# Optimization experiments

Measured on AMD Instinct MI355X. Metric: run time of the kernel, lower is better.

Reference implementation:

```python
import jax, jax.numpy as jnp
import numpy as np

B, S, H = 2, 2048, 4096
NH, HD = 32, 128          # num attention heads, head dim (kv_channels)
KVH = 2                   # multi_query_group_num (KV heads)
ROT = HD // 2             # 64 rotary dims -> rope cache last-2 dim = 32
QKV = NH * HD + 2 * KVH * HD  # 4608


def apply_rope(x, rope):
    # x: [b, nh, s, hd]; rope: [b, s, ROT//2, 2]
    b, nh, s, hd = x.shape
    x_rot, x_pass = x[..., :ROT], x[..., ROT:]
    xs = x_rot.reshape(b, nh, s, ROT // 2, 2)
    rc = rope[:, :s].reshape(b, 1, s, ROT // 2, 2)
    out = jnp.stack([
        xs[..., 0] * rc[..., 0] - xs[..., 1] * rc[..., 1],
        xs[..., 1] * rc[..., 0] + xs[..., 0] * rc[..., 1],
    ], axis=-1).reshape(b, nh, s, ROT)
    return jnp.concatenate([out, x_pass], axis=-1)


def setup_inputs() -> dict:
    key = jax.random.key(0)
    ks = jax.random.split(key, 6)
    hidden_states = jax.random.normal(ks[0], (B, S, H), dtype=jnp.float32)
    rotary_pos_emb = jax.random.normal(ks[1], (B, S, ROT // 2, 2), dtype=jnp.float32)
    # causal mask: True = masked (strict upper triangle), matching module's ~tril
    causal = jnp.triu(jnp.ones((S, S), dtype=jnp.bool_), k=1)
    attention_mask = jnp.broadcast_to(causal[None, None], (B, 1, S, S))
    W_qkv = jax.random.normal(ks[2], (QKV, H), dtype=jnp.float32) * (1.0 / np.sqrt(H))
    b_qkv = jax.random.normal(ks[3], (QKV,), dtype=jnp.float32) * 0.02
    W_dense = jax.random.normal(ks[4], (H, NH * HD), dtype=jnp.float32) * (1.0 / np.sqrt(NH * HD))
    return {"hidden_states": hidden_states, "rotary_pos_emb": rotary_pos_emb,
            "attention_mask": attention_mask, "W_qkv": W_qkv, "b_qkv": b_qkv,
            "W_dense": W_dense}


def reference(hidden_states, rotary_pos_emb, attention_mask, W_qkv, b_qkv, W_dense):
    b, s, _ = hidden_states.shape
    mixed = hidden_states @ W_qkv.T + b_qkv  # [b, s, QKV]
    q, k, v = jnp.split(mixed, [NH * HD, NH * HD + KVH * HD], axis=-1)
    q = q.reshape(b, s, NH, HD).transpose(0, 2, 1, 3)   # [b, NH, s, hd]
    k = k.reshape(b, s, KVH, HD).transpose(0, 2, 1, 3)  # [b, KVH, s, hd]
    v = v.reshape(b, s, KVH, HD).transpose(0, 2, 1, 3)
    q = apply_rope(q, rotary_pos_emb)
    k = apply_rope(k, rotary_pos_emb)
    # GQA expand KV heads to NH
    rep = NH // KVH
    k = jnp.repeat(k, rep, axis=1)
    v = jnp.repeat(v, rep, axis=1)
    scale = 1.0 / np.sqrt(HD)
    scores = jnp.einsum('bhqd,bhkd->bhqk', q, k).astype(jnp.float32) * scale
    scores = jnp.where(attention_mask, -jnp.inf, scores)
    probs = jax.nn.softmax(scores, axis=-1).astype(v.dtype)
    ctx = jnp.einsum('bhqk,bhkd->bhqd', probs, v)       # [b, NH, s, hd]
    ctx = ctx.transpose(0, 2, 1, 3).reshape(b, s, NH * HD)
    return ctx @ W_dense.T
```

## Files before the change

### kernel.cpp

```cpp
#include <hip/hip_runtime.h>
#include <hip/hip_bf16.h>
#include <stdint.h>

#define Bb 2
#define Ss 2048
#define Hh 4096
#define NHh 32
#define HDd 128
#define KVHh 2

typedef __attribute__((ext_vector_type(8))) short bf16x8;
typedef __attribute__((ext_vector_type(4))) float f32x4;
typedef __attribute__((ext_vector_type(16))) float f32x16;
typedef __attribute__((ext_vector_type(4))) unsigned int u32x4;
typedef unsigned short u16;
typedef unsigned int u32;
typedef unsigned long long u64;

__device__ __forceinline__ u16 f2b(float f) {
  union { float f; u32 u; } v; v.f = f;
  u32 r = v.u + 0x7fffu + ((v.u >> 16) & 1u);
  return (u16)(r >> 16);
}
__device__ __forceinline__ float b2f(u16 h) {
  union { u32 u; float f; } v; v.u = ((u32)h) << 16;
  return v.f;
}

__device__ __forceinline__ u32 cvtpk(float lo, float hi_) {
  u32 r;
  asm("v_cvt_pk_bf16_f32 %0, %1, %2" : "=v"(r) : "v"(lo), "v"(hi_));
  return r;
}
__device__ __forceinline__ void plswap(u32& x, u32& y) {
  asm volatile("v_permlane32_swap_b32 %0, %1" : "+v"(x), "+v"(y));
}

__device__ __forceinline__ void gload_lds16(const u16* g, u16* l) {
  __builtin_amdgcn_global_load_lds(
      (const __attribute__((address_space(1))) u32*)(uintptr_t)g,
      (__attribute__((address_space(3))) u32*)(u32)(uintptr_t)l,
      16, 0, 0);
}

__global__ void cvt2_k(const float* __restrict__ a, u16* __restrict__ oa,
                       const float* __restrict__ b, u16* __restrict__ ob) {
  int i = blockIdx.x * blockDim.x + threadIdx.x;
  const float* src;
  u16* dst;
  int off;
  if (i < 4194304) { src = a; dst = oa; off = i; }
  else { src = b; dst = ob; off = i - 4194304; }
  int idx = off * 4;
  float4 v = *(const float4*)&src[idx];
  u64 pack = (u64)f2b(v.x) | ((u64)f2b(v.y) << 16) |
             ((u64)f2b(v.z) << 32) | ((u64)f2b(v.w) << 48);
  *(u64*)&dst[idx] = pack;
}

__global__ void cvtW_k(const float* __restrict__ in, u16* __restrict__ out) {
  int i = blockIdx.x * blockDim.x + threadIdx.x;
  int idx = i * 4;
  float4 v = *(const float4*)&in[idx];
  u64 pack = (u64)f2b(v.x) | ((u64)f2b(v.y) << 16) |
             ((u64)f2b(v.z) << 32) | ((u64)f2b(v.w) << 48);
  *(u64*)&out[idx] = pack;
}

__global__ void rope_k(u16* __restrict__ X, const float* __restrict__ rope, int nheads) {
  int i = blockIdx.x * blockDim.x + threadIdx.x;
  int p = i & 31;
  int s = (i >> 5) & (Ss - 1);
  int bh = i >> 16;
  if (bh >= Bb * nheads) return;
  int b = bh / nheads;
  size_t base = ((size_t)bh * Ss + s) * HDd + p * 2;
  u32 x01 = *(u32*)&X[base];
  float x0 = b2f((u16)(x01 & 0xffff));
  float x1 = b2f((u16)(x01 >> 16));
  float2 rc = *(const float2*)&rope[(((size_t)b * Ss + s) * 32 + p) * 2];
  float o0 = x0 * rc.x - x1 * rc.y;
  float o1 = x1 * rc.x + x0 * rc.y;
  u32 o = (u32)f2b(o0) | ((u32)f2b(o1) << 16);
  *(u32*)&X[base] = o;
}

template <int KK>
__device__ __forceinline__ void stage_tileA(const u16* __restrict__ gbase, u16* dst, int tid) {
#pragma unroll
  for (int li = 0; li < 2; ++li) {
    int t16 = li * 512 + tid;
    int rt = t16 >> 2, ct = t16 & 3;
    int cg = ct ^ ((rt >> 1) & 3);
    gload_lds16(gbase + (size_t)rt * KK + cg * 8, dst + t16 * 8);
  }
}
template <int KK>
__device__ __forceinline__ void stage_tileB(const u16* __restrict__ gbase, u16* dst, int tid) {
  int t16 = tid;
  int rt = t16 >> 2, ct = t16 & 3;
  int cg = ct ^ ((rt >> 1) & 3);
  gload_lds16(gbase + (size_t)rt * KK + cg * 8, dst + t16 * 8);
}

__device__ __forceinline__ bf16x8 frag128(const u16* buf, int row, int lk) {
  int ch = lk ^ ((row >> 1) & 3);
  return *(const bf16x8*)&buf[row * 32 + ch * 8];
}

template <int NN, int KK, int COLG>
__global__ __launch_bounds__(512, 4) void gemm_qkv(
    const u16* __restrict__ A, const u16* __restrict__ Bm,
    const float* __restrict__ bias,
    u16* __restrict__ Qb, u16* __restrict__ Kb, u16* __restrict__ Vb) {
  __shared__ u16 As[2][8192];
  __shared__ u16 Bs[2][4096];
  const int tid = threadIdx.x;
  const int wave = tid >> 6;
  const int lane = tid & 63;
  const int lr = lane & 15;
  const int lk = lane >> 4;
  const int wr = wave >> 1;
  const int wc = wave & 1;
  const int bid = blockIdx.x;
  const int xcd = bid & 7;
  const int local = bid >> 3;
  const int rlr = local / COLG;
  const int rlc = local - rlr * COLG;
  const int m0 = ((xcd >> 2) * 8 + rlr) * 256;
  const int n0 = ((xcd & 3) * COLG + rlc) * 128;
  const int NT = KK / 32;

  f32x4 acc[4][4];
#pragma unroll
  for (int i = 0; i < 4; ++i)
#pragma unroll
    for (int j = 0; j < 4; ++j) acc[i][j] = (f32x4){0.f, 0.f, 0.f, 0.f};

  const u16* Ab = A + (size_t)m0 * KK;
  const u16* Bw = Bm + (size_t)n0 * KK;

  stage_tileA<KK>(Ab, &As[0][0], tid);
  stage_tileB<KK>(Bw, &Bs[0][0], tid);
  asm volatile("s_waitcnt vmcnt(0)");
  __syncthreads();

  int cur = 0;
  for (int t = 0; t < NT; ++t) {
    if (t + 1 < NT) {
      stage_tileA<KK>(Ab + (t + 1) * 32, &As[cur ^ 1][0], tid);
      stage_tileB<KK>(Bw + (t + 1) * 32, &Bs[cur ^ 1][0], tid);
      asm volatile("s_waitcnt vmcnt(3)");
    } else {
      asm volatile("s_waitcnt vmcnt(0)");
    }
    __builtin_amdgcn_s_barrier();
    __builtin_amdgcn_sched_barrier(0);

    bf16x8 af[4], bf[4];
#pragma unroll
    for (int mi = 0; mi < 4; ++mi)
      af[mi] = frag128(&As[cur][0], wr * 64 + mi * 16 + lr, lk);
#pragma unroll
    for (int ni = 0; ni < 4; ++ni)
      bf[ni] = frag128(&Bs[cur][0], wc * 64 + ni * 16 + lr, lk);
    asm volatile("s_waitcnt lgkmcnt(0)");
    __builtin_amdgcn_sched_barrier(0);
    __builtin_amdgcn_s_setprio(1);
#pragma unroll
    for (int mi = 0; mi < 4; ++mi)
#pragma unroll
      for (int ni = 0; ni < 4; ++ni)
        acc[mi][ni] = __builtin_amdgcn_mfma_f32_16x16x32_bf16(af[mi], bf[ni], acc[mi][ni], 0, 0, 0);
    __builtin_amdgcn_s_setprio(0);
    __builtin_amdgcn_s_barrier();
    cur ^= 1;
  }

#pragma unroll
  for (int ni = 0; ni < 4; ++ni) {
    int n = n0 + wc * 64 + ni * 16 + lr;
    float bv = bias[n];
#pragma unroll
    for (int mi = 0; mi < 4; ++mi) {
      int mb = m0 + wr * 64 + mi * 16 + lk * 4;
#pragma unroll
      for (int j = 0; j < 4; ++j) {
        int m = mb + j;
        int bb = m >> 11;
        int ss = m & 2047;
        u16 hv = f2b(acc[mi][ni][j] + bv);
        if (n < 4096) {
          Qb[(((size_t)bb * NHh + (n >> 7)) * Ss + ss) * HDd + (n & 127)] = hv;
        } else if (n < 4352) {
          int idx2 = n - 4096;
          Kb[(((size_t)bb * KVHh + (idx2 >> 7)) * Ss + ss) * HDd + (idx2 & 127)] = hv;
        } else {
          int idx2 = n - 4352;
          Vb[(((size_t)bb * KVHh + (idx2 >> 7)) * Ss + ss) * HDd + (idx2 & 127)] = hv;
        }
      }
    }
  }
}

__global__ __launch_bounds__(512, 2) void gemm_d256(
    const u16* __restrict__ A, const u16* __restrict__ Bm,
    float* __restrict__ Cout) {
  __shared__ u16 SM[2][4][8192];
  const int tid = threadIdx.x;
  const int wave = tid >> 6;
  const int lane = tid & 63;
  const int lr = lane & 15;
  const int lk = lane >> 4;
  const int wr = wave >> 2;
  const int wc = wave & 3;
  const int bid = blockIdx.x;
  const int xcd = bid & 7;
  const int local = bid >> 3;
  const int m0 = ((xcd >> 2) * 8 + (local >> 2)) * 256;
  const int n0 = ((xcd & 3) * 4 + (local & 3)) * 256;
  const int NT = 64;

  f32x4 acc[8][4];
#pragma unroll
  for (int i = 0; i < 8; ++i)
#pragma unroll
    for (int j = 0; j < 4; ++j) acc[i][j] = (f32x4){0.f, 0.f, 0.f, 0.f};

  auto stage_half = [&](const u16* grows, int j, u16* dst) {
    if (j >= NT) return;
#pragma unroll
    for (int li = 0; li < 2; ++li) {
      int t16 = li * 512 + tid;
      int row = t16 >> 3, c = t16 & 7;
      int cs = c ^ (row & 7);
      gload_lds16(grows + (size_t)row * 4096 + j * 64 + cs * 8, dst + t16 * 8);
    }
  };
  const u16* Ah0g = A + (size_t)m0 * 4096;
  const u16* Ah1g = A + (size_t)(m0 + 128) * 4096;
  const u16* Bh0g = Bm + (size_t)n0 * 4096;
  const u16* Bh1g = Bm + (size_t)(n0 + 128) * 4096;

  stage_half(Ah0g, 0, &SM[0][2][0]);
  stage_half(Ah1g, 0, &SM[0][3][0]);
  stage_half(Bh0g, 0, &SM[0][0][0]);
  stage_half(Bh1g, 0, &SM[0][1][0]);
  stage_half(Bh0g, 1, &SM[1][0][0]);
  stage_half(Bh1g, 1, &SM[1][1][0]);
  asm volatile("s_waitcnt vmcnt(0)");
  __builtin_amdgcn_s_barrier();
  __builtin_amdgcn_sched_barrier(0);

  for (int kt = 0; kt < NT; ++kt) {
    const int cur = kt & 1;
    const int nxt = cur ^ 1;
    const u16* Ahl = &SM[cur][2 + wr][0];
    const u16* Bhl = &SM[cur][wc >> 1][0];
    const int rB0 = (wc & 1) * 64;
    auto rdA = [&](int r, int kk) {
      int ch = (kk * 4 + lk) ^ (r & 7);
      return *(const bf16x8*)&Ahl[r * 64 + ch * 8];
    };
    auto rdB = [&](int r, int kk) {
      int ch = (kk * 4 + lk) ^ (r & 7);
      return *(const bf16x8*)&Bhl[r * 64 + ch * 8];
    };

    bf16x8 bfr[4][2], af[2][2];
#pragma unroll
    for (int ni = 0; ni < 4; ++ni)
#pragma unroll
      for (int kk = 0; kk < 2; ++kk)
        bfr[ni][kk] = rdB(rB0 + ni * 16 + lr, kk);
#pragma unroll
    for (int i = 0; i < 2; ++i)
#pragma unroll
      for (int kk = 0; kk < 2; ++kk)
        af[i][kk] = rdA(i * 16 + lr, kk);
    stage_half(Ah0g, kt + 1, &SM[nxt][2][0]);
    __builtin_amdgcn_s_barrier();
    asm volatile("s_waitcnt lgkmcnt(0)");
    __builtin_amdgcn_sched_barrier(0);
    __builtin_amdgcn_s_setprio(1);
#pragma unroll
    for (int i = 0; i < 2; ++i)
#pragma unroll
      for (int ni = 0; ni < 4; ++ni)
#pragma unroll
        for (int kk = 0; kk < 2; ++kk)
          acc[i][ni] = __builtin_amdgcn_mfma_f32_16x16x32_bf16(af[i][kk], bfr[ni][kk], acc[i][ni], 0, 0, 0);
    __builtin_amdgcn_s_setprio(0);
    __builtin_amdgcn_s_barrier();

#pragma unroll
    for (int i = 0; i < 2; ++i)
#pragma unroll
      for (int kk = 0; kk < 2; ++kk)
        af[i][kk] = rdA((2 + i) * 16 + lr, kk);
    stage_half(Ah1g, kt + 1, &SM[nxt][3][0]);
    __builtin_amdgcn_s_barrier();
    asm volatile("s_waitcnt lgkmcnt(0)");
    __builtin_amdgcn_sched_barrier(0);
    __builtin_amdgcn_s_setprio(1);
#pragma unroll
    for (int i = 0; i < 2; ++i)
#pragma unroll
      for (int ni = 0; ni < 4; ++ni)
#pragma unroll
        for (int kk = 0; kk < 2; ++kk)
          acc[2 + i][ni] = __builtin_amdgcn_mfma_f32_16x16x32_bf16(af[i][kk], bfr[ni][kk], acc[2 + i][ni], 0, 0, 0);
    __builtin_amdgcn_s_setprio(0);
    __builtin_amdgcn_s_barrier();

#pragma unroll
    for (int i = 0; i < 2; ++i)
#pragma unroll
      for (int kk = 0; kk < 2; ++kk)
        af[i][kk] = rdA((4 + i) * 16 + lr, kk);
    stage_half(Bh0g, kt + 2, &SM[cur][0][0]);
    __builtin_amdgcn_s_barrier();
    asm volatile("s_waitcnt lgkmcnt(0)");
    __builtin_amdgcn_sched_barrier(0);
    __builtin_amdgcn_s_setprio(1);
#pragma unroll
    for (int i = 0; i < 2; ++i)
#pragma unroll
      for (int ni = 0; ni < 4; ++ni)
#pragma unroll
        for (int kk = 0; kk < 2; ++kk)
          acc[4 + i][ni] = __builtin_amdgcn_mfma_f32_16x16x32_bf16(af[i][kk], bfr[ni][kk], acc[4 + i][ni], 0, 0, 0);
    __builtin_amdgcn_s_setprio(0);
    __builtin_amdgcn_s_barrier();

#pragma unroll
    for (int i = 0; i < 2; ++i)
#pragma unroll
      for (int kk = 0; kk < 2; ++kk)
        af[i][kk] = rdA((6 + i) * 16 + lr, kk);
    stage_half(Bh1g, kt + 2, &SM[cur][1][0]);
    __builtin_amdgcn_s_barrier();
    asm volatile("s_waitcnt lgkmcnt(0)");
    __builtin_amdgcn_sched_barrier(0);
    __builtin_amdgcn_s_setprio(1);
#pragma unroll
    for (int i = 0; i < 2; ++i)
#pragma unroll
      for (int ni = 0; ni < 4; ++ni)
#pragma unroll
        for (int kk = 0; kk < 2; ++kk)
          acc[6 + i][ni] = __builtin_amdgcn_mfma_f32_16x16x32_bf16(af[i][kk], bfr[ni][kk], acc[6 + i][ni], 0, 0, 0);
    __builtin_amdgcn_s_setprio(0);
    if (kt < NT - 2) {
      asm volatile("s_waitcnt vmcnt(4)");
    } else {
      asm volatile("s_waitcnt vmcnt(0)");
    }
    __builtin_amdgcn_s_barrier();
    __builtin_amdgcn_sched_barrier(0);
  }

#pragma unroll
  for (int mi = 0; mi < 8; ++mi)
#pragma unroll
    for (int ni = 0; ni < 4; ++ni) {
      int col = n0 + wc * 64 + ni * 16 + lr;
      int rowb = m0 + wr * 128 + mi * 16 + lk * 4;
#pragma unroll
      for (int j = 0; j < 4; ++j)
        Cout[(size_t)(rowb + j) * 4096 + col] = acc[mi][ni][j];
    }
}

__global__ __launch_bounds__(512, 2) void attn_k(
    const u16* __restrict__ Qb, const u16* __restrict__ Kb,
    const u16* __restrict__ Vb, const float* __restrict__ rope,
    u16* __restrict__ Ctx) {
  __shared__ u16 Kt[2][64 * 128];
  __shared__ u16 Vt[2][128 * 64];
  const int tid = threadIdx.x;
  const int w = tid >> 6;
  const int lane = tid & 63;
  const int l31 = lane & 31;
  const int hi = lane >> 5;
  const int h = blockIdx.y, b = blockIdx.z;
  const int hkv = h >> 4;
  const u16* Qp = Qb + ((size_t)(b * NHh + h)) * Ss * HDd;
  const u16* Kp = Kb + ((size_t)(b * KVHh + hkv)) * Ss * HDd;
  const u16* Vp = Vb + ((size_t)(b * KVHh + hkv)) * Ss * HDd;

  const float scale = 0.08838834764831845f;
  const float L2E = 1.4426950408889634f;

  for (int hp = 0; hp < 2; ++hp) {
    const int qt = hp == 0 ? (7 - (int)blockIdx.x) : (int)blockIdx.x;
    const int qs = qt * 256;
    const int qw = qs + w * 32;
    const int qrow = qw + l31;
    const int nt = qs / 64 + 4;

    bf16x8 qf[8];
#pragma unroll
    for (int ds = 0; ds < 8; ++ds)
      qf[ds] = *(const bf16x8*)&Qp[(size_t)qrow * HDd + ds * 16 + hi * 8];
#pragma unroll
    for (int ds = 0; ds < 4; ++ds) {
      bf16x8 q = qf[ds];
      bf16x8 o;
#pragma unroll
      for (int i = 0; i < 4; ++i) {
        int p = ds * 8 + hi * 4 + i;
        float2 rc = *(const float2*)&rope[(((size_t)b * Ss + qrow) * 32 + p) * 2];
        float x0 = b2f((u16)q[2 * i]), x1 = b2f((u16)q[2 * i + 1]);
        o[2 * i] = (short)f2b(x0 * rc.x - x1 * rc.y);
        o[2 * i + 1] = (short)f2b(x1 * rc.x + x0 * rc.y);
      }
      qf[ds] = o;
    }

    f32x16 accO[4];
#pragma unroll
    for (int i = 0; i < 4; ++i)
#pragma unroll
      for (int r = 0; r < 16; ++r) accO[i][r] = 0.f;
    float m_r = -3.0e38f, l_r = 0.f;

    {
#pragma unroll
      for (int i = 0; i < 2; ++i) {
        int slot = w * 2 + i;
        int r = slot * 4 + (lane >> 4);
        int p = lane & 15;
        int gc = (p & 8) | ((p ^ r) & 7);
        gload_lds16(Kp + (size_t)r * HDd + gc * 8, &Kt[0][slot * 512]);
      }
      bf16x8 v0 = *(const bf16x8*)&Vp[(size_t)lane * HDd + w * 16];
      bf16x8 v1 = *(const bf16x8*)&Vp[(size_t)lane * HDd + w * 16 + 8];
      u32x4 sv = __builtin_bit_cast(u32x4, (lane & 1) ? v0 : v1);
      u32x4 rv;
      rv.x = __shfl_xor(sv.x, 1); rv.y = __shfl_xor(sv.y, 1);
      rv.z = __shfl_xor(sv.z, 1); rv.w = __shfl_xor(sv.w, 1);
      bf16x8 recv = __builtin_bit_cast(bf16x8, rv);
      int kvp = lane >> 1;
#pragma unroll
      for (int i = 0; i < 8; ++i) {
        int d = w * 16 + (lane & 1) * 8 + i;
        u16 lo = (lane & 1) ? (u16)recv[i] : (u16)v0[i];
        u16 hb = (lane & 1) ? (u16)v1[i] : (u16)recv[i];
        u32 val = (u32)lo | ((u32)hb << 16);
        int cp = (kvp >> 2) ^ (d & 7);
        *(u32*)&Vt[0][d * 64 + cp * 8 + (kvp & 3) * 2] = val;
      }
    }
    __syncthreads();

    for (int t = 0; t < nt; ++t) {
      const int j0 = t * 64;
      const int cur = t & 1;
      const bool havenext = (t + 1 < nt);
      bf16x8 nv0, nv1;
      if (havenext) {
        const int j1 = j0 + 64;
#pragma unroll
        for (int i = 0; i < 2; ++i) {
          int slot = w * 2 + i;
          int r = slot * 4 + (lane >> 4);
          int p = lane & 15;
          int gc = (p & 8) | ((p ^ r) & 7);
          gload_lds16(Kp + (size_t)(j1 + r) * HDd + gc * 8, &Kt[cur ^ 1][slot * 512]);
        }
        nv0 = *(const bf16x8*)&Vp[(size_t)(j1 + lane) * HDd + w * 16];
        nv1 = *(const bf16x8*)&Vp[(size_t)(j1 + lane) * HDd + w * 16 + 8];
      }

      if (j0 <= qw + 31) {
        f32x16 aS[2];
#pragma unroll
        for (int a = 0; a < 2; ++a)
#pragma unroll
          for (int r = 0; r < 16; ++r) aS[a][r] = 0.f;
#pragma unroll
        for (int kvb = 0; kvb < 2; ++kvb) {
          int r = kvb * 32 + l31;
#pragma unroll
          for (int ds = 0; ds < 8; ++ds) {
            int c = ds * 2 + hi;
            int cp = (c & 8) | ((c ^ r) & 7);
            bf16x8 kf = *(const bf16x8*)&Kt[cur][r * 128 + cp * 8];
            aS[kvb] = __builtin_amdgcn_mfma_f32_32x32x16_bf16(kf, qf[ds], aS[kvb], 0, 0, 0);
          }
        }
        const bool needmask = (j0 + 63 > qw);
        float mx = -3.0e38f;
#pragma unroll
        for (int a = 0; a < 2; ++a)
#pragma unroll
          for (int r = 0; r < 16; ++r) {
            float s = aS[a][r] * scale;
            if (needmask) {
              int kv = j0 + a * 32 + (r & 3) + 8 * (r >> 2) + 4 * hi;
              s = (kv > qrow) ? -3.0e38f : s;
            }
            aS[a][r] = s;
            mx = fmaxf(mx, s);
          }
        mx = fmaxf(mx, __shfl_xor(mx, 32));
        if (!__all(mx - m_r <= 8.0f)) {
          float mnew = fmaxf(m_r, mx);
          float corr = __builtin_amdgcn_exp2f((m_r - mnew) * L2E);
          l_r *= corr;
#pragma unroll
          for (int i = 0; i < 4; ++i)
#pragma unroll
            for (int r = 0; r < 16; ++r) accO[i][r] *= corr;
          m_r = mnew;
        }
        float sum = 0.f;
#pragma unroll
        for (int a = 0; a < 2; ++a)
#pragma unroll
          for (int r = 0; r < 16; ++r) {
            float pe = __builtin_amdgcn_exp2f((aS[a][r] - m_r) * L2E);
            aS[a][r] = pe;
            sum += pe;
          }
        sum += __shfl_xor(sum, 32);
        l_r += sum;

        u32 cc0[2][4], cc1[2][4];
#pragma unroll
        for (int a = 0; a < 2; ++a)
#pragma unroll
          for (int g = 0; g < 4; ++g) {
            cc0[a][g] = cvtpk(aS[a][g * 4 + 0], aS[a][g * 4 + 1]);
            cc1[a][g] = cvtpk(aS[a][g * 4 + 2], aS[a][g * 4 + 3]);
          }
        bf16x8 pa[4];
#pragma unroll
        for (int ks = 0; ks < 4; ++ks) {
          int a = ks >> 1, g0 = (ks & 1) * 2;
          u32 w0 = cc0[a][g0], w2 = cc0[a][g0 + 1];
          u32 w1 = cc1[a][g0], w3 = cc1[a][g0 + 1];
          plswap(w0, w2);
          plswap(w1, w3);
          u32x4 tv; tv.x = w0; tv.y = w1; tv.z = w2; tv.w = w3;
          pa[ks] = __builtin_bit_cast(bf16x8, tv);
        }
#pragma unroll
        for (int dblk = 0; dblk < 4; ++dblk) {
          int d = dblk * 32 + l31;
#pragma unroll
          for (int ks = 0; ks < 4; ++ks) {
            int c = ks * 2 + hi;
            int cp = c ^ (d & 7);
            bf16x8 vf = *(const bf16x8*)&Vt[cur][d * 64 + cp * 8];
            accO[dblk] = __builtin_amdgcn_mfma_f32_32x32x16_bf16(vf, pa[ks], accO[dblk], 0, 0, 0);
          }
        }
      }

      if (havenext) {
        u32x4 sv = __builtin_bit_cast(u32x4, (lane & 1) ? nv0 : nv1);
        u32x4 rv;
        rv.x = __shfl_xor(sv.x, 1); rv.y = __shfl_xor(sv.y, 1);
        rv.z = __shfl_xor(sv.z, 1); rv.w = __shfl_xor(sv.w, 1);
        bf16x8 recv = __builtin_bit_cast(bf16x8, rv);
        int kvp = lane >> 1;
#pragma unroll
        for (int i = 0; i < 8; ++i) {
          int d = w * 16 + (lane & 1) * 8 + i;
          u16 lo = (lane & 1) ? (u16)recv[i] : (u16)nv0[i];
          u16 hb = (lane & 1) ? (u16)nv1[i] : (u16)recv[i];
          u32 val = (u32)lo | ((u32)hb << 16);
          int cp = (kvp >> 2) ^ (d & 7);
          *(u32*)&Vt[cur ^ 1][d * 64 + cp * 8 + (kvp & 3) * 2] = val;
        }
      }
      __syncthreads();
    }

    {
      float il = 1.0f / l_r;
      size_t rb = ((size_t)b * Ss + qrow) * (size_t)(NHh * HDd) + (size_t)h * HDd;
#pragma unroll
      for (int dblk = 0; dblk < 4; ++dblk)
#pragma unroll
        for (int g = 0; g < 4; ++g) {
          int d0 = dblk * 32 + g * 8 + hi * 4;
          u64 pack = (u64)f2b(accO[dblk][g * 4 + 0] * il) |
                     ((u64)f2b(accO[dblk][g * 4 + 1] * il) << 16) |
                     ((u64)f2b(accO[dblk][g * 4 + 2] * il) << 32) |
                     ((u64)f2b(accO[dblk][g * 4 + 3] * il) << 48);
          *(u64*)&Ctx[rb + d0] = pack;
        }
    }
    __syncthreads();
  }
}

extern "C" void kernel_launch(void* const* d_in, const int* in_sizes, int n_in,
                              void* d_out, int out_size, void* d_ws, size_t ws_size,
                              hipStream_t stream) {
  const float* hidden = (const float*)d_in[0];
  const float* rope = (const float*)d_in[1];
  const float* Wqkv = (const float*)d_in[3];
  const float* bqkv = (const float*)d_in[4];
  const float* Wdense = (const float*)d_in[5];
  float* out = (float*)d_out;

  char* w = (char*)d_ws;
  u16* Xbf = (u16*)w;
  u16* ctx = Xbf;
  w += (size_t)33554432;
  u16* Wq = (u16*)w;
  u16* Wd = Wq;
  w += (size_t)37748736;
  u16* Qb = (u16*)w; w += (size_t)33554432;
  u16* Kb = (u16*)w; w += (size_t)2097152;
  u16* Vb = (u16*)w; w += (size_t)2097152;

  cvt2_k<<<34816, 256, 0, stream>>>(hidden, Xbf, Wqkv, Wq);
  gemm_qkv<4608, 4096, 9><<<dim3(576), 512, 0, stream>>>(
      Xbf, Wq, bqkv, Qb, Kb, Vb);
  rope_k<<<(Bb * KVHh * Ss * 32 + 255) / 256, 256, 0, stream>>>(Kb, rope, KVHh);
  cvtW_k<<<16384, 256, 0, stream>>>(Wdense, Wd);
  attn_k<<<dim3(4, NHh, Bb), 512, 0, stream>>>(Qb, Kb, Vb, rope, ctx);
  gemm_d256<<<dim3(256), 512, 0, stream>>>(ctx, Wd, out);
}
```

Before: 471.6 us.

## Replace QKV GEMM with 256x256 tiled kernel folding KV columns into Q tiles

The QKV projection GEMM moves from 256x128 tiles over 576 blocks to 256x256 tiles over 256 blocks, reusing the same schedule as the dense GEMM. It uses 64-wide K steps with four-phase interleaved staging and a larger accumulator. The 512 K/V output columns are split into 32-column slices, and each Q tile computes one slice as an extra small MFMA product in a side accumulator. The aim is more data reuse per load and a launch that fits exactly one wave of blocks, at the cost of more registers, lower occupancy and more complex wait-count bookkeeping.

```diff
diff --git a/kernel.cpp b/kernel.cpp
--- a/kernel.cpp
+++ b/kernel.cpp
@@ -85,96 +85,211 @@
   *(u32*)&X[base] = o;
 }
 
-template <int KK>
-__device__ __forceinline__ void stage_tileA(const u16* __restrict__ gbase, u16* dst, int tid) {
-#pragma unroll
-  for (int li = 0; li < 2; ++li) {
-    int t16 = li * 512 + tid;
-    int rt = t16 >> 2, ct = t16 & 3;
-    int cg = ct ^ ((rt >> 1) & 3);
-    gload_lds16(gbase + (size_t)rt * KK + cg * 8, dst + t16 * 8);
-  }
-}
-template <int KK>
-__device__ __forceinline__ void stage_tileB(const u16* __restrict__ gbase, u16* dst, int tid) {
-  int t16 = tid;
-  int rt = t16 >> 2, ct = t16 & 3;
-  int cg = ct ^ ((rt >> 1) & 3);
-  gload_lds16(gbase + (size_t)rt * KK + cg * 8, dst + t16 * 8);
-}
-
-__device__ __forceinline__ bf16x8 frag128(const u16* buf, int row, int lk) {
-  int ch = lk ^ ((row >> 1) & 3);
-  return *(const bf16x8*)&buf[row * 32 + ch * 8];
-}
-
-template <int NN, int KK, int COLG>
-__global__ __launch_bounds__(512, 4) void gemm_qkv(
+__global__ __launch_bounds__(512, 2) void gemm_qkv256(
     const u16* __restrict__ A, const u16* __restrict__ Bm,
     const float* __restrict__ bias,
     u16* __restrict__ Qb, u16* __restrict__ Kb, u16* __restrict__ Vb) {
-  __shared__ u16 As[2][8192];
-  __shared__ u16 Bs[2][4096];
+  __shared__ u16 SM[2][4][8192];
+  __shared__ u16 BKV[2][4096];
   const int tid = threadIdx.x;
   const int wave = tid >> 6;
   const int lane = tid & 63;
   const int lr = lane & 15;
   const int lk = lane >> 4;
-  const int wr = wave >> 1;
-  const int wc = wave & 1;
+  const int wr = wave >> 2;
+  const int wc = wave & 3;
   const int bid = blockIdx.x;
   const int xcd = bid & 7;
   const int local = bid >> 3;
-  const int rlr = local / COLG;
-  const int rlc = local - rlr * COLG;
-  const int m0 = ((xcd >> 2) * 8 + rlr) * 256;
-  const int n0 = ((xcd & 3) * COLG + rlc) * 128;
-  const int NT = KK / 32;
-
-  f32x4 acc[4][4];
-#pragma unroll
-  for (int i = 0; i < 4; ++i)
+  const int m0 = ((xcd >> 2) * 8 + (local >> 2)) * 256;
+  const int ntile = (xcd & 3) * 4 + (local & 3);
+  const int n0 = ntile * 256;
+  const int NT = 64;
+
+  f32x4 acc[8][4];
+#pragma unroll
+  for (int i = 0; i < 8; ++i)
 #pragma unroll
     for (int j = 0; j < 4; ++j) acc[i][j] = (f32x4){0.f, 0.f, 0.f, 0.f};
-
-  const u16* Ab = A + (size_t)m0 * KK;
-  const u16* Bw = Bm + (size_t)n0 * KK;
-
-  stage_tileA<KK>(Ab, &As[0][0], tid);
-  stage_tileB<KK>(Bw, &Bs[0][0], tid);
+  f32x4 acckv[2][2];
+#pragma unroll
+  for (int i = 0; i < 2; ++i)
+#pragma unroll
+    for (int j = 0; j < 2; ++j) acckv[i][j] = (f32x4){0.f, 0.f, 0.f, 0.f};
+
+  auto stage_half = [&](const u16* grows, int j, u16* dst) {
+    if (j >= NT) return;
+#pragma unroll
+    for (int li = 0; li < 2; ++li) {
+      int t16 = li * 512 + tid;
+      int row = t16 >> 3, c = t16 & 7;
+      int cs = c ^ (row & 7);
+      gload_lds16(grows + (size_t)row * 4096 + j * 64 + cs * 8, dst + t16 * 8);
+    }
+  };
+  const u16* Ah0g = A + (size_t)m0 * 4096;
+  const u16* Ah1g = A + (size_t)(m0 + 128) * 4096;
+  const u16* Bh0g = Bm + (size_t)n0 * 4096;
+  const u16* Bh1g = Bm + (size_t)(n0 + 128) * 4096;
+  const u16* KVg = Bm + (size_t)(4096 + ntile * 32) * 4096;
+
+  auto stage_bkv = [&](int j2) {
+    if (j2 >= NT) return;
+    int sub = tid >> 8;
+    int idx = tid & 255;
+    int row = idx >> 3, c = idx & 7;
+    int cs = c ^ (row & 7);
+    gload_lds16(KVg + (size_t)row * 4096 + (j2 + sub) * 64 + cs * 8,
+                &BKV[(j2 >> 1) & 1][sub * 2048] + idx * 8);
+  };
+
+  stage_half(Ah0g, 0, &SM[0][2][0]);
+  stage_half(Ah1g, 0, &SM[0][3][0]);
+  stage_half(Bh0g, 0, &SM[0][0][0]);
+  stage_half(Bh1g, 0, &SM[0][1][0]);
+  stage_half(Bh0g, 1, &SM[1][0][0]);
+  stage_half(Bh1g, 1, &SM[1][1][0]);
+  stage_bkv(0);
   asm volatile("s_waitcnt vmcnt(0)");
-  __syncthreads();
-
-  int cur = 0;
-  for (int t = 0; t < NT; ++t) {
-    if (t + 1 < NT) {
-      stage_tileA<KK>(Ab + (t + 1) * 32, &As[cur ^ 1][0], tid);
-      stage_tileB<KK>(Bw + (t + 1) * 32, &Bs[cur ^ 1][0], tid);
-      asm volatile("s_waitcnt vmcnt(3)");
+  __builtin_amdgcn_s_barrier();
+  __builtin_amdgcn_sched_barrier(0);
+
+  for (int kt = 0; kt < NT; ++kt) {
+    const int cur = kt & 1;
+    const int nxt = cur ^ 1;
+    const u16* Ahl = &SM[cur][2 + wr][0];
+    const u16* Bhl = &SM[cur][wc >> 1][0];
+    const u16* Bkvl = &BKV[(kt >> 1) & 1][(kt & 1) * 2048];
+    const int rB0 = (wc & 1) * 64;
+    auto rdA = [&](int r, int kk) {
+      int ch = (kk * 4 + lk) ^ (r & 7);
+      return *(const bf16x8*)&Ahl[r * 64 + ch * 8];
+    };
+    auto rdB = [&](int r, int kk) {
+      int ch = (kk * 4 + lk) ^ (r & 7);
+      return *(const bf16x8*)&Bhl[r * 64 + ch * 8];
+    };
+    auto rdBkv = [&](int r, int kk) {
+      int ch = (kk * 4 + lk) ^ (r & 7);
+      return *(const bf16x8*)&Bkvl[r * 64 + ch * 8];
+    };
+
+    bf16x8 bfr[4][2], af[2][2];
+#pragma unroll
+    for (int ni = 0; ni < 4; ++ni)
+#pragma unroll
+      for (int kk = 0; kk < 2; ++kk)
+        bfr[ni][kk] = rdB(rB0 + ni * 16 + lr, kk);
+#pragma unroll
+    for (int i = 0; i < 2; ++i)
+#pragma unroll
+      for (int kk = 0; kk < 2; ++kk)
+        af[i][kk] = rdA(i * 16 + lr, kk);
+    stage_half(Ah0g, kt + 1, &SM[nxt][2][0]);
+    __builtin_amdgcn_s_barrier();
+    asm volatile("s_waitcnt lgkmcnt(0)");
+    __builtin_amdgcn_sched_barrier(0);
+    __builtin_amdgcn_s_setprio(1);
+#pragma unroll
+    for (int i = 0; i < 2; ++i)
+#pragma unroll
+      for (int ni = 0; ni < 4; ++ni)
+#pragma unroll
+        for (int kk = 0; kk < 2; ++kk)
+          acc[i][ni] = __builtin_amdgcn_mfma_f32_16x16x32_bf16(af[i][kk], bfr[ni][kk], acc[i][ni], 0, 0, 0);
+    __builtin_amdgcn_s_setprio(0);
+    __builtin_amdgcn_s_barrier();
+
+    {
+      bf16x8 afkv[2][2], bfkv[2][2];
+#pragma unroll
+      for (int i = 0; i < 2; ++i)
+#pragma unroll
+        for (int kk = 0; kk < 2; ++kk)
+          af[i][kk] = rdA((2 + i) * 16 + lr, kk);
+#pragma unroll
+      for (int rg = 0; rg < 2; ++rg)
+#pragma unroll
+        for (int kk = 0; kk < 2; ++kk)
+          afkv[rg][kk] = rdA(wc * 32 + rg * 16 + lr, kk);
+#pragma unroll
+      for (int cg = 0; cg < 2; ++cg)
+#pragma unroll
+        for (int kk = 0; kk < 2; ++kk)
+          bfkv[cg][kk] = rdBkv(cg * 16 + lr, kk);
+      stage_half(Ah1g, kt + 1, &SM[nxt][3][0]);
+      if ((kt & 1) == 0) stage_bkv(kt + 2);
+      __builtin_amdgcn_s_barrier();
+      asm volatile("s_waitcnt lgkmcnt(0)");
+      __builtin_amdgcn_sched_barrier(0);
+      __builtin_amdgcn_s_setprio(1);
+#pragma unroll
+      for (int i = 0; i < 2; ++i)
+#pragma unroll
+        for (int ni = 0; ni < 4; ++ni)
+#pragma unroll
+          for (int kk = 0; kk < 2; ++kk)
+            acc[2 + i][ni] = __builtin_amdgcn_mfma_f32_16x16x32_bf16(af[i][kk], bfr[ni][kk], acc[2 + i][ni], 0, 0, 0);
+#pragma unroll
+      for (int rg = 0; rg < 2; ++rg)
+#pragma unroll
+        for (int cg = 0; cg < 2; ++cg)
+#pragma unroll
+          for (int kk = 0; kk < 2; ++kk)
+            acckv[rg][cg] = __builtin_amdgcn_mfma_f32_16x16x32_bf16(afkv[rg][kk], bfkv[cg][kk], acckv[rg][cg], 0, 0, 0);
+      __builtin_amdgcn_s_setprio(0);
+      __builtin_amdgcn_s_barrier();
+    }
+
+#pragma unroll
+    for (int i = 0; i < 2; ++i)
+#pragma unroll
+      for (int kk = 0; kk < 2; ++kk)
+        af[i][kk] = rdA((4 + i) * 16 + lr, kk);
+    stage_half(Bh0g, kt + 2, &SM[cur][0][0]);
+    __builtin_amdgcn_s_barrier();
+    asm volatile("s_waitcnt lgkmcnt(0)");
+    __builtin_amdgcn_sched_barrier(0);
+    __builtin_amdgcn_s_setprio(1);
+#pragma unroll
+    for (int i = 0; i < 2; ++i)
+#pragma unroll
+      for (int ni = 0; ni < 4; ++ni)
+#pragma unroll
+        for (int kk = 0; kk < 2; ++kk)
+          acc[4 + i][ni] = __builtin_amdgcn_mfma_f32_16x16x32_bf16(af[i][kk], bfr[ni][kk], acc[4 + i][ni], 0, 0, 0);
+    __builtin_amdgcn_s_setprio(0);
+    __builtin_amdgcn_s_barrier();
+
+#pragma unroll
+    for (int i = 0; i < 2; ++i)
+#pragma unroll
+      for (int kk = 0; kk < 2; ++kk)
+        af[i][kk] = rdA((6 + i) * 16 + lr, kk);
+    stage_half(Bh1g, kt + 2, &SM[cur][1][0]);
+    __builtin_amdgcn_s_barrier();
+    asm volatile("s_waitcnt lgkmcnt(0)");
+    __builtin_amdgcn_sched_barrier(0);
+    __builtin_amdgcn_s_setprio(1);
+#pragma unroll
+    for (int i = 0; i < 2; ++i)
+#pragma unroll
+      for (int ni = 0; ni < 4; ++ni)
+#pragma unroll
+        for (int kk = 0; kk < 2; ++kk)
+          acc[6 + i][ni] = __builtin_amdgcn_mfma_f32_16x16x32_bf16(af[i][kk], bfr[ni][kk], acc[6 + i][ni], 0, 0, 0);
+    __builtin_amdgcn_s_setprio(0);
+    if (kt < NT - 2) {
+      if ((kt & 1) == 0) {
+        asm volatile("s_waitcnt vmcnt(5)");
+      } else {
+        asm volatile("s_waitcnt vmcnt(4)");
+      }
     } else {
       asm volatile("s_waitcnt vmcnt(0)");
     }
     __builtin_amdgcn_s_barrier();
     __builtin_amdgcn_sched_barrier(0);
-
-    bf16x8 af[4], bf[4];
-#pragma unroll
-    for (int mi = 0; mi < 4; ++mi)
-      af[mi] = frag128(&As[cur][0], wr * 64 + mi * 16 + lr, lk);
-#pragma unroll
-    for (int ni = 0; ni < 4; ++ni)
-      bf[ni] = frag128(&Bs[cur][0], wc * 64 + ni * 16 + lr, lk);
-    asm volatile("s_waitcnt lgkmcnt(0)");
-    __builtin_amdgcn_sched_barrier(0);
-    __builtin_amdgcn_s_setprio(1);
-#pragma unroll
-    for (int mi = 0; mi < 4; ++mi)
-#pragma unroll
-      for (int ni = 0; ni < 4; ++ni)
-        acc[mi][ni] = __builtin_amdgcn_mfma_f32_16x16x32_bf16(af[mi], bf[ni], acc[mi][ni], 0, 0, 0);
-    __builtin_amdgcn_s_setprio(0);
-    __builtin_amdgcn_s_barrier();
-    cur ^= 1;
   }
 
 #pragma unroll
@@ -182,26 +297,38 @@
     int n = n0 + wc * 64 + ni * 16 + lr;
     float bv = bias[n];
 #pragma unroll
-    for (int mi = 0; mi < 4; ++mi) {
-      int mb = m0 + wr * 64 + mi * 16 + lk * 4;
+    for (int mi = 0; mi < 8; ++mi) {
+      int mb = m0 + wr * 128 + mi * 16 + lk * 4;
 #pragma unroll
       for (int j = 0; j < 4; ++j) {
         int m = mb + j;
         int bb = m >> 11;
         int ss = m & 2047;
         u16 hv = f2b(acc[mi][ni][j] + bv);
-        if (n < 4096) {
-          Qb[(((size_t)bb * NHh + (n >> 7)) * Ss + ss) * HDd + (n & 127)] = hv;
-        } else if (n < 4352) {
-          int idx2 = n - 4096;
-          Kb[(((size_t)bb * KVHh + (idx2 >> 7)) * Ss + ss) * HDd + (idx2 & 127)] = hv;
+        Qb[(((size_t)bb * NHh + (n >> 7)) * Ss + ss) * HDd + (n & 127)] = hv;
+      }
+    }
+  }
+#pragma unroll
+  for (int rg = 0; rg < 2; ++rg)
+#pragma unroll
+    for (int cg = 0; cg < 2; ++cg) {
+      int kvcol = ntile * 32 + cg * 16 + lr;
+      float bv = bias[4096 + kvcol];
+#pragma unroll
+      for (int j = 0; j < 4; ++j) {
+        int m = m0 + wr * 128 + wc * 32 + rg * 16 + lk * 4 + j;
+        int bb = m >> 11;
+        int ss = m & 2047;
+        u16 hv = f2b(acckv[rg][cg][j] + bv);
+        if (kvcol < 256) {
+          Kb[(((size_t)bb * KVHh + (kvcol >> 7)) * Ss + ss) * HDd + (kvcol & 127)] = hv;
         } else {
-          int idx2 = n - 4352;
-          Vb[(((size_t)bb * KVHh + (idx2 >> 7)) * Ss + ss) * HDd + (idx2 & 127)] = hv;
+          int i2 = kvcol - 256;
+          Vb[(((size_t)bb * KVHh + (i2 >> 7)) * Ss + ss) * HDd + (i2 & 127)] = hv;
         }
       }
     }
-  }
 }
 
 __global__ __launch_bounds__(512, 2) void gemm_d256(
@@ -621,8 +748,7 @@
   u16* Vb = (u16*)w; w += (size_t)2097152;
 
   cvt2_k<<<34816, 256, 0, stream>>>(hidden, Xbf, Wqkv, Wq);
-  gemm_qkv<4608, 4096, 9><<<dim3(576), 512, 0, stream>>>(
-      Xbf, Wq, bqkv, Qb, Kb, Vb);
+  gemm_qkv256<<<dim3(256), 512, 0, stream>>>(Xbf, Wq, bqkv, Qb, Kb, Vb);
   rope_k<<<(Bb * KVHh * Ss * 32 + 255) / 256, 256, 0, stream>>>(Kb, rope, KVHh);
   cvtW_k<<<16384, 256, 0, stream>>>(Wdense, Wd);
   attn_k<<<dim3(4, NHh, Bb), 512, 0, stream>>>(Qb, Kb, Vb, rope, ctx);
```

Measured after the change: 413.3 us. -12.4%, faster.
